# Kernel tuning notes

Hardware: AMD Instinct MI355X
Metric: run time of the kernel (lower is better)

The kernel has to match this reference:

```python
import jax, jax.numpy as jnp
import numpy as np

T, L, D, P, H = 1024, 32, 512, 512, 2048
EPS = 1e-5  # torch LayerNorm default eps


def _layer_norm(x, g, b):
    m = x.mean(axis=-1, keepdims=True)
    v = ((x - m) ** 2).mean(axis=-1, keepdims=True)
    return (x - m) * jax.lax.rsqrt(v + EPS) * g + b


def setup_inputs() -> dict:
    key = jax.random.key(0)
    ks = jax.random.split(key, 16)
    s = 0.02
    inp = {
        "base_prompts": jax.random.normal(ks[0], (T, L, D), jnp.float32),
        "new_prompt": jax.random.normal(ks[1], (L, D), jnp.float32),
        "task_embedding": jax.random.normal(ks[2], (D,), jnp.float32),
        # linear weights stored (in, out) so forward is x @ W + b
        "Wt": jax.random.normal(ks[3], (D, P), jnp.float32) * s,
        "bt": jnp.zeros((P,), jnp.float32),
        "Wq": jax.random.normal(ks[4], (D, P), jnp.float32) * s,
        "bq": jnp.zeros((P,), jnp.float32),
        "Wk": jax.random.normal(ks[5], (D, P), jnp.float32) * s,
        "bk": jnp.zeros((P,), jnp.float32),
        "Wv": jax.random.normal(ks[6], (D, P), jnp.float32) * s,
        "bv": jnp.zeros((P,), jnp.float32),
        "Wo": jax.random.normal(ks[7], (P, D), jnp.float32) * s,
        "bo": jnp.zeros((D,), jnp.float32),
        "Wa1": jax.random.normal(ks[8], (D, H), jnp.float32) * s,
        "ba1": jnp.zeros((H,), jnp.float32),
        "Wa2": jax.random.normal(ks[9], (H, D), jnp.float32) * s,
        "ba2": jnp.zeros((D,), jnp.float32),
        "g_in": jnp.ones((D,), jnp.float32),
        "b_in": jnp.zeros((D,), jnp.float32),
        "g_out": jnp.ones((D,), jnp.float32),
        "b_out": jnp.zeros((D,), jnp.float32),
    }
    return inp


def reference(base_prompts, new_prompt, task_embedding,
              Wt, bt, Wq, bq, Wk, bk, Wv, bv, Wo, bo,
              Wa1, ba1, Wa2, ba2, g_in, b_in, g_out, b_out):
    scale = 1.0 / np.sqrt(P).astype(np.float32)

    # --- task conditioning ---
    task_vec = jnp.tanh(task_embedding @ Wt + bt)                 # [P]
    key_repr = (base_prompts @ Wk + bk).mean(axis=1)              # [T,P]
    scores = (key_repr @ task_vec) * scale                        # [T]
    task_weights = jax.nn.softmax(scores)
    conditioned = base_prompts * (1.0 + task_weights[:, None, None])  # [T,L,D]

    query = new_prompt @ Wq + bq                                  # [L,P]
    keys = conditioned @ Wk + bk                                  # [T,L,P]
    values = conditioned @ Wv + bv                                # [T,L,P]

    # --- task-level attention ---
    pooled_q = query.mean(axis=0)                                 # [P]
    pooled_k = keys.mean(axis=1)                                  # [T,P]
    task_attn = jax.nn.softmax((pooled_k @ pooled_q) * scale)     # [T]
    task_weights = 0.5 * task_weights + 0.5 * task_attn
    task_weights = task_weights / jnp.maximum(task_weights.sum(), 1e-6)

    # --- enhanced mode: weighted pooling over tasks ---
    weighted_values = jnp.einsum('t,tlp->lp', task_weights, values)       # [L,P]
    weighted_keys = jnp.einsum('t,tlp->lp', task_weights, keys)           # [L,P]
    weighted_prompts = jnp.einsum('t,tld->ld', task_weights, conditioned) # [L,D]

    # --- feature-level attention ---
    feature_logits = (query @ weighted_keys.T) * scale            # [L,L]
    feature_attn = jax.nn.softmax(feature_logits, axis=-1)
    evolved_proj = feature_attn @ weighted_values                 # [L,P]

    evolved = evolved_proj @ Wo + bo                              # [L,D]
    evolved = _layer_norm(weighted_prompts + evolved, g_in, b_in)
    mlp = jax.nn.relu(evolved @ Wa1 + ba1) @ Wa2 + ba2
    aligned = _layer_norm(evolved + mlp, g_out, b_out)            # [L,D]

    aligned_prompts = jnp.broadcast_to(aligned, (T, L, D))        # stack of identical aligned prompts
    return aligned, aligned_prompts, task_weights, feature_attn
```

## Files before the change

### kernel.cpp

```cpp
#include <hip/hip_runtime.h>


typedef unsigned int u32;

static constexpr int T_ = 1024, L_ = 32, D_ = 512, P_ = 512, H_ = 2048;
static constexpr float SCALE = 0.04419417382415922f;
static constexpr float EPS_ = 1e-5f;

static constexpr int OFF_QUERY   = 0;
static constexpr int OFF_TV      = 16384;
static constexpr int OFF_PQ      = 16896;
static constexpr int OFF_WKTV    = 17408;
static constexpr int OFF_WKPQ    = 17920;
static constexpr int OFF_U       = 18432;
static constexpr int OFF_V       = 19456;
static constexpr int OFF_C       = 20480;
static constexpr int OFF_PART    = 21504;
static constexpr int OFF_WBASE   = 545792;
static constexpr int OFF_WKEY    = 562176;
static constexpr int OFF_WVAL    = 578560;
static constexpr int OFF_FA      = 594944;
static constexpr int OFF_EP      = 595968;
static constexpr int OFF_EVOLVED = 612352;
static constexpr int OFF_AQ      = 628736;
static constexpr int OFF_AKV     = 645632;
static constexpr int OFF_AEVO    = 678400;
static constexpr int OFF_AH1     = 694784;
static constexpr int OFF_AOUT    = 760320;
static constexpr int ZERO_BEGIN  = OFF_AQ;
static constexpr int ZERO_F4     = (776704 - 628736) / 4;

static constexpr int OFFO_AL = 0;
static constexpr int OFFO_AP = 16384;
static constexpr int OFFO_TW = 16384 + 16777216;
static constexpr int OFFO_FA = OFFO_TW + 1024;

__device__ __forceinline__ float wred(float v) {
    #pragma unroll
    for (int off = 32; off > 0; off >>= 1) v += __shfl_down(v, off, 64);
    return v;
}
template <int NT>
__device__ __forceinline__ float fsum(float v, float* buf, int tid) {
    v = wred(v);
    if ((tid & 63) == 0) buf[tid >> 6] = v;
    __syncthreads();
    if (tid == 0) { float s = 0.f; for (int i = 0; i < NT / 64; ++i) s += buf[i]; buf[0] = s; }
    __syncthreads();
    float r = buf[0]; __syncthreads();
    return r;
}
template <int NT>
__device__ __forceinline__ float fmaxr(float v, float* buf, int tid) {
    #pragma unroll
    for (int off = 32; off > 0; off >>= 1) v = fmaxf(v, __shfl_down(v, off, 64));
    if ((tid & 63) == 0) buf[tid >> 6] = v;
    __syncthreads();
    if (tid == 0) { float s = buf[0]; for (int i = 1; i < NT / 64; ++i) s = fmaxf(s, buf[i]); buf[0] = s; }
    __syncthreads();
    float r = buf[0]; __syncthreads();
    return r;
}

__global__ void k_zero(float* __restrict__ ws) {
    int i = blockIdx.x * 256 + threadIdx.x;
    if (i < ZERO_F4) ((float4*)(ws + ZERO_BEGIN))[i] = make_float4(0.f, 0.f, 0.f, 0.f);
}

__global__ void k_query_g(const float* __restrict__ np, const float* __restrict__ te,
                          const float* __restrict__ Wq, const float* __restrict__ Wt,
                          float* __restrict__ ws) {
    __shared__ float sx[128];
    int p = threadIdx.x, b = blockIdx.x, kc = blockIdx.y;
    const float* x = (b < L_) ? (np + b * D_) : te;
    if (p < 128) sx[p] = x[kc * 128 + p];
    __syncthreads();
    const float* W = (b < L_) ? Wq : Wt;
    float acc = 0.f;
    #pragma unroll 8
    for (int j = 0; j < 128; ++j) acc = fmaf(sx[j], W[(kc * 128 + j) * P_ + p], acc);
    atomicAdd(&ws[OFF_AQ + b * P_ + p], acc);
}

__global__ void k_query_ep(const float* __restrict__ bq, const float* __restrict__ bt,
                           float* __restrict__ ws) {
    int p = threadIdx.x, b = blockIdx.x;
    if (b < L_) ws[OFF_QUERY + b * P_ + p] = ws[OFF_AQ + b * P_ + p] + bq[p];
    else        ws[OFF_TV + p] = tanhf(ws[OFF_AQ + L_ * P_ + p] + bt[p]);
}

__global__ void k_pq(float* __restrict__ ws) {
    int p = threadIdx.x;
    float s = 0.f;
    for (int l = 0; l < L_; ++l) s += ws[OFF_QUERY + l * P_ + p];
    ws[OFF_PQ + p] = s * (1.0f / L_);
}

__global__ void k_wk2(const float* __restrict__ Wk, float* __restrict__ ws) {
    int tid = threadIdx.x, wv = tid >> 6, lane = tid & 63;
    int d = blockIdx.x * 8 + wv;
    const float4* row = (const float4*)(Wk + d * P_);
    const float4* tv4 = (const float4*)(ws + OFF_TV);
    const float4* pq4 = (const float4*)(ws + OFF_PQ);
    float4 a = row[lane * 2], b = row[lane * 2 + 1];
    float4 t0 = tv4[lane * 2], t1 = tv4[lane * 2 + 1];
    float4 q0 = pq4[lane * 2], q1 = pq4[lane * 2 + 1];
    float pa = a.x * t0.x + a.y * t0.y + a.z * t0.z + a.w * t0.w
             + b.x * t1.x + b.y * t1.y + b.z * t1.z + b.w * t1.w;
    float pb = a.x * q0.x + a.y * q0.y + a.z * q0.z + a.w * q0.w
             + b.x * q1.x + b.y * q1.y + b.z * q1.z + b.w * q1.w;
    pa = wred(pa); pb = wred(pb);
    if (lane == 0) { ws[OFF_WKTV + d] = pa; ws[OFF_WKPQ + d] = pb; }
}

__global__ void k_bbar(const float* __restrict__ base, float* __restrict__ ws) {
    __shared__ float buf[8];
    int t = blockIdx.x, d = threadIdx.x;
    const float* bp = base + (size_t)t * (L_ * D_);
    float s = 0.f;
    for (int l = 0; l < L_; ++l) s += bp[l * D_ + d];
    float up = fsum<512>(s * ws[OFF_WKTV + d], buf, d);
    float vp = fsum<512>(s * ws[OFF_WKPQ + d], buf, d);
    if (d == 0) {
        ws[OFF_U + t] = up * (1.0f / L_);
        ws[OFF_V + t] = vp * (1.0f / L_);
    }
}

__global__ void k_soft(const float* __restrict__ bk, float* __restrict__ out_tw,
                       float* __restrict__ ws) {
    __shared__ float buf[8];
    int tid = threadIdx.x;
    float pbt = 0.f, pbq = 0.f;
    for (int p = tid; p < P_; p += 256) {
        float bkf = bk[p];
        pbt = fmaf(bkf, ws[OFF_TV + p], pbt);
        pbq = fmaf(bkf, ws[OFF_PQ + p], pbq);
    }
    float bkt = fsum<256>(pbt, buf, tid);
    float bkq = fsum<256>(pbq, buf, tid);

    float s1[4], e1[4], tw1[4], lmax = -1e30f;
    #pragma unroll
    for (int k = 0; k < 4; ++k) {
        s1[k] = (ws[OFF_U + tid + k * 256] + bkt) * SCALE;
        lmax = fmaxf(lmax, s1[k]);
    }
    float gmax = fmaxr<256>(lmax, buf, tid);
    float ls = 0.f;
    #pragma unroll
    for (int k = 0; k < 4; ++k) { e1[k] = expf(s1[k] - gmax); ls += e1[k]; }
    float gs = fsum<256>(ls, buf, tid);
    #pragma unroll
    for (int k = 0; k < 4; ++k) tw1[k] = e1[k] / gs;

    float p2[4], e2[4];
    lmax = -1e30f;
    #pragma unroll
    for (int k = 0; k < 4; ++k) {
        p2[k] = ((1.0f + tw1[k]) * ws[OFF_V + tid + k * 256] + bkq) * SCALE;
        lmax = fmaxf(lmax, p2[k]);
    }
    gmax = fmaxr<256>(lmax, buf, tid);
    ls = 0.f;
    #pragma unroll
    for (int k = 0; k < 4; ++k) { e2[k] = expf(p2[k] - gmax); ls += e2[k]; }
    gs = fsum<256>(ls, buf, tid);

    float tw[4], lsum = 0.f;
    #pragma unroll
    for (int k = 0; k < 4; ++k) { tw[k] = 0.5f * tw1[k] + 0.5f * (e2[k] / gs); lsum += tw[k]; }
    float S = fsum<256>(lsum, buf, tid);
    S = fmaxf(S, 1e-6f);
    #pragma unroll
    for (int k = 0; k < 4; ++k) {
        int t = tid + k * 256;
        float twn = tw[k] / S;
        out_tw[t] = twn;
        ws[OFF_C + t] = twn * (1.0f + tw1[k]);
    }
}

__global__ void k_wpart(const float* __restrict__ base, float* __restrict__ ws) {
    __shared__ float cs[32];
    int l = blockIdx.x, ch = blockIdx.y, tid = threadIdx.x;
    if (tid < 32) cs[tid] = ws[OFF_C + ch * 32 + tid];
    __syncthreads();
    float a0 = 0.f, a1 = 0.f, a2 = 0.f, a3 = 0.f;
    for (int i = 0; i < 32; ++i) {
        int t = ch * 32 + i;
        float4 v = ((const float4*)(base + ((size_t)t * L_ + l) * D_))[tid];
        float cc = cs[i];
        a0 = fmaf(cc, v.x, a0); a1 = fmaf(cc, v.y, a1);
        a2 = fmaf(cc, v.z, a2); a3 = fmaf(cc, v.w, a3);
    }
    ((float4*)(ws + OFF_PART + (ch * L_ + l) * D_))[tid] = make_float4(a0, a1, a2, a3);
}

__global__ void k_wred(float* __restrict__ ws) {
    int l = blockIdx.x, d = threadIdx.x;
    float s = 0.f;
    for (int ch = 0; ch < 32; ++ch) s += ws[OFF_PART + (ch * L_ + l) * D_ + d];
    ws[OFF_WBASE + l * D_ + d] = s;
}

__global__ void k_wkv_g(const float* __restrict__ Wk, const float* __restrict__ Wv,
                        float* __restrict__ ws) {
    __shared__ float sx[128];
    int p = threadIdx.x, l = blockIdx.x, sel = blockIdx.y, kc = blockIdx.z;
    if (p < 128) sx[p] = ws[OFF_WBASE + l * D_ + kc * 128 + p];
    __syncthreads();
    const float* W = sel ? Wv : Wk;
    float acc = 0.f;
    #pragma unroll 8
    for (int j = 0; j < 128; ++j) acc = fmaf(sx[j], W[(kc * 128 + j) * P_ + p], acc);
    atomicAdd(&ws[OFF_AKV + (sel * L_ + l) * P_ + p], acc);
}

__global__ void k_wkv_ep(const float* __restrict__ bk, const float* __restrict__ bv,
                         float* __restrict__ ws) {
    int p = threadIdx.x, l = blockIdx.x, sel = blockIdx.y;
    float b = sel ? bv[p] : bk[p];
    ws[(sel ? OFF_WVAL : OFF_WKEY) + l * P_ + p] = ws[OFF_AKV + (sel * L_ + l) * P_ + p] + b;
}

__global__ void k_logits(float* __restrict__ out_fa, float* __restrict__ ws) {
    __shared__ __align__(16) float sq[512];
    __shared__ float lg[32];
    int l = blockIdx.x, tid = threadIdx.x, wv = tid >> 6, lane = tid & 63;
    sq[tid] = ws[OFF_QUERY + l * P_ + tid];
    __syncthreads();
    const float4* sq4 = (const float4*)sq;
    float4 q0 = sq4[lane * 2], q1 = sq4[lane * 2 + 1];
    for (int g = wv * 4; g < wv * 4 + 4; ++g) {
        const float4* kr = (const float4*)(ws + OFF_WKEY + g * P_);
        float4 a = kr[lane * 2], b = kr[lane * 2 + 1];
        float s = a.x * q0.x + a.y * q0.y + a.z * q0.z + a.w * q0.w
                + b.x * q1.x + b.y * q1.y + b.z * q1.z + b.w * q1.w;
        s = wred(s);
        if (lane == 0) lg[g] = s * SCALE;
    }
    __syncthreads();
    if (tid < 32) {
        float mx = -1e30f;
        for (int i = 0; i < 32; ++i) mx = fmaxf(mx, lg[i]);
        float S = 0.f;
        for (int i = 0; i < 32; ++i) S += expf(lg[i] - mx);
        float f = expf(lg[tid] - mx) / S;
        ws[OFF_FA + l * 32 + tid] = f;
        out_fa[l * 32 + tid] = f;
    }
}

__global__ void k_ep(float* __restrict__ ws) {
    __shared__ float fa[32];
    int l = blockIdx.x, p = threadIdx.x;
    if (p < 32) fa[p] = ws[OFF_FA + l * 32 + p];
    __syncthreads();
    float acc = 0.f;
    #pragma unroll 8
    for (int j = 0; j < L_; ++j) acc = fmaf(fa[j], ws[OFF_WVAL + j * P_ + p], acc);
    ws[OFF_EP + l * P_ + p] = acc;
}

__global__ void k_evo_g(const float* __restrict__ Wo, float* __restrict__ ws) {
    __shared__ float sx[128];
    int d = threadIdx.x, l = blockIdx.x, kc = blockIdx.y;
    if (d < 128) sx[d] = ws[OFF_EP + l * P_ + kc * 128 + d];
    __syncthreads();
    float acc = 0.f;
    #pragma unroll 8
    for (int j = 0; j < 128; ++j) acc = fmaf(sx[j], Wo[(kc * 128 + j) * D_ + d], acc);
    atomicAdd(&ws[OFF_AEVO + l * D_ + d], acc);
}

__global__ void k_xin_ln(const float* __restrict__ bo, const float* __restrict__ g_in,
                         const float* __restrict__ b_in, float* __restrict__ ws) {
    __shared__ float buf[8];
    int l = blockIdx.x, d = threadIdx.x;
    float x = ws[OFF_WBASE + l * D_ + d] + ws[OFF_AEVO + l * D_ + d] + bo[d];
    float mean = fsum<512>(x, buf, d) * (1.0f / D_);
    float dx = x - mean;
    float var = fsum<512>(dx * dx, buf, d) * (1.0f / D_);
    ws[OFF_EVOLVED + l * D_ + d] = dx * rsqrtf(var + EPS_) * g_in[d] + b_in[d];
}

__global__ void k_mlp1_g(const float* __restrict__ Wa1, float* __restrict__ ws) {
    __shared__ float sx[128];
    int tid = threadIdx.x, l = blockIdx.x, hc = blockIdx.y, kc = blockIdx.z;
    if (tid < 128) sx[tid] = ws[OFF_EVOLVED + l * D_ + kc * 128 + tid];
    __syncthreads();
    int h = hc * 512 + tid;
    float acc = 0.f;
    #pragma unroll 8
    for (int j = 0; j < 128; ++j) acc = fmaf(sx[j], Wa1[(kc * 128 + j) * H_ + h], acc);
    atomicAdd(&ws[OFF_AH1 + l * H_ + h], acc);
}

__global__ void k_mlp2_g(const float* __restrict__ Wa2, const float* __restrict__ ba1,
                         float* __restrict__ ws) {
    __shared__ float sh[128];
    int d = threadIdx.x, l = blockIdx.x, kc = blockIdx.y;
    if (d < 128) {
        int h = kc * 128 + d;
        sh[d] = fmaxf(ws[OFF_AH1 + l * H_ + h] + ba1[h], 0.f);
    }
    __syncthreads();
    float acc = 0.f;
    #pragma unroll 8
    for (int j = 0; j < 128; ++j) acc = fmaf(sh[j], Wa2[(kc * 128 + j) * D_ + d], acc);
    atomicAdd(&ws[OFF_AOUT + l * D_ + d], acc);
}

__global__ void k_lnout(const float* __restrict__ ba2, const float* __restrict__ g_out,
                        const float* __restrict__ b_out, float* __restrict__ out_al,
                        float* __restrict__ ws) {
    __shared__ float buf[8];
    int l = blockIdx.x, d = threadIdx.x;
    float x = ws[OFF_EVOLVED + l * D_ + d] + ws[OFF_AOUT + l * D_ + d] + ba2[d];
    float mean = fsum<512>(x, buf, d) * (1.0f / D_);
    float dx = x - mean;
    float var = fsum<512>(dx * dx, buf, d) * (1.0f / D_);
    out_al[l * D_ + d] = dx * rsqrtf(var + EPS_) * g_out[d] + b_out[d];
}

__global__ void k_bcast(float* __restrict__ out) {
    const float4* src = (const float4*)out;
    float4* dst = (float4*)(out + OFFO_AP);
    int idx = blockIdx.x * 256 + threadIdx.x;
    #pragma unroll
    for (int k = 0; k < 4; ++k) {
        int v = idx + k * 1048576;
        dst[v] = src[v & 4095];
    }
}

extern "C" void kernel_launch(void* const* d_in, const int* in_sizes, int n_in,
                              void* d_out, int out_size, void* d_ws, size_t ws_size,
                              hipStream_t stream) {
    const float* base = (const float*)d_in[0];
    const float* np   = (const float*)d_in[1];
    const float* te   = (const float*)d_in[2];
    const float* Wt   = (const float*)d_in[3];
    const float* bt   = (const float*)d_in[4];
    const float* Wq   = (const float*)d_in[5];
    const float* bq   = (const float*)d_in[6];
    const float* Wk   = (const float*)d_in[7];
    const float* bk   = (const float*)d_in[8];
    const float* Wv   = (const float*)d_in[9];
    const float* bv   = (const float*)d_in[10];
    const float* Wo   = (const float*)d_in[11];
    const float* bo   = (const float*)d_in[12];
    const float* Wa1  = (const float*)d_in[13];
    const float* ba1  = (const float*)d_in[14];
    const float* Wa2  = (const float*)d_in[15];
    const float* ba2  = (const float*)d_in[16];
    const float* g_in = (const float*)d_in[17];
    const float* b_in = (const float*)d_in[18];
    const float* g_out= (const float*)d_in[19];
    const float* b_out= (const float*)d_in[20];
    float* out = (float*)d_out;
    float* ws = out + OFFO_AP;

    hipLaunchKernelGGL(k_zero,     dim3(145),        dim3(256), 0, stream, ws);
    hipLaunchKernelGGL(k_query_g,  dim3(33, 4),      dim3(512), 0, stream, np, te, Wq, Wt, ws);
    hipLaunchKernelGGL(k_query_ep, dim3(33),         dim3(512), 0, stream, bq, bt, ws);
    hipLaunchKernelGGL(k_pq,       dim3(1),          dim3(512), 0, stream, ws);
    hipLaunchKernelGGL(k_wk2,      dim3(64),         dim3(512), 0, stream, Wk, ws);
    hipLaunchKernelGGL(k_bbar,     dim3(1024),       dim3(512), 0, stream, base, ws);
    hipLaunchKernelGGL(k_soft,     dim3(1),          dim3(256), 0, stream, bk, out + OFFO_TW, ws);
    hipLaunchKernelGGL(k_wpart,    dim3(32, 32),     dim3(128), 0, stream, base, ws);
    hipLaunchKernelGGL(k_wred,     dim3(32),         dim3(512), 0, stream, ws);
    hipLaunchKernelGGL(k_wkv_g,    dim3(32, 2, 4),   dim3(512), 0, stream, Wk, Wv, ws);
    hipLaunchKernelGGL(k_wkv_ep,   dim3(32, 2),      dim3(512), 0, stream, bk, bv, ws);
    hipLaunchKernelGGL(k_logits,   dim3(32),         dim3(512), 0, stream, out + OFFO_FA, ws);
    hipLaunchKernelGGL(k_ep,       dim3(32),         dim3(512), 0, stream, ws);
    hipLaunchKernelGGL(k_evo_g,    dim3(32, 4),      dim3(512), 0, stream, Wo, ws);
    hipLaunchKernelGGL(k_xin_ln,   dim3(32),         dim3(512), 0, stream, bo, g_in, b_in, ws);
    hipLaunchKernelGGL(k_mlp1_g,   dim3(32, 4, 4),   dim3(512), 0, stream, Wa1, ws);
    hipLaunchKernelGGL(k_mlp2_g,   dim3(32, 16),     dim3(512), 0, stream, Wa2, ba1, ws);
    hipLaunchKernelGGL(k_lnout,    dim3(32),         dim3(512), 0, stream, ba2, g_out, b_out, out + OFFO_AL, ws);
    hipLaunchKernelGGL(k_bcast,    dim3(4096),       dim3(256), 0, stream, out);
}
```

Before: 254.5 us.

## Fuse all stages into one cooperative persistent kernel with grid syncs

Replaces the chain of nineteen small kernel launches with a single cooperative kernel of 256 blocks that runs every stage in turn, separated by grid.sync. Atomics and the zeroing kernel go away because each GEMV block now owns its full reduction. Several stages are merged (bias folding, logits with value pooling, out-projection and layernorm), and the base-prompt sum is overlapped with the query GEMV. The aim is to cut launch overhead and inter-kernel gaps. In exchange, the small stages leave most blocks idle between grid barriers, and the large bandwidth-bound stages run on only 256 blocks.

```diff
diff --git a/kernel.cpp b/kernel.cpp
--- a/kernel.cpp
+++ b/kernel.cpp
@@ -1,337 +1,371 @@
 #include <hip/hip_runtime.h>
-
-
-typedef unsigned int u32;
+#include <hip/hip_cooperative_groups.h>
+
+
+namespace cg = cooperative_groups;
 
 static constexpr int T_ = 1024, L_ = 32, D_ = 512, P_ = 512, H_ = 2048;
 static constexpr float SCALE = 0.04419417382415922f;
 static constexpr float EPS_ = 1e-5f;
-
-static constexpr int OFF_QUERY   = 0;
-static constexpr int OFF_TV      = 16384;
-static constexpr int OFF_PQ      = 16896;
-static constexpr int OFF_WKTV    = 17408;
-static constexpr int OFF_WKPQ    = 17920;
-static constexpr int OFF_U       = 18432;
-static constexpr int OFF_V       = 19456;
-static constexpr int OFF_C       = 20480;
-static constexpr int OFF_PART    = 21504;
-static constexpr int OFF_WBASE   = 545792;
-static constexpr int OFF_WKEY    = 562176;
-static constexpr int OFF_WVAL    = 578560;
-static constexpr int OFF_FA      = 594944;
-static constexpr int OFF_EP      = 595968;
-static constexpr int OFF_EVOLVED = 612352;
-static constexpr int OFF_AQ      = 628736;
-static constexpr int OFF_AKV     = 645632;
-static constexpr int OFF_AEVO    = 678400;
-static constexpr int OFF_AH1     = 694784;
-static constexpr int OFF_AOUT    = 760320;
-static constexpr int ZERO_BEGIN  = OFF_AQ;
-static constexpr int ZERO_F4     = (776704 - 628736) / 4;
+static constexpr int NB = 256;
+static constexpr int NT = 512;
 
 static constexpr int OFFO_AL = 0;
 static constexpr int OFFO_AP = 16384;
 static constexpr int OFFO_TW = 16384 + 16777216;
 static constexpr int OFFO_FA = OFFO_TW + 1024;
 
-__device__ __forceinline__ float wred(float v) {
+static constexpr int OFF_SB      = 0;
+static constexpr int OFF_AQ      = 524288;
+static constexpr int OFF_QUERY   = 541184;
+static constexpr int OFF_TV      = 557568;
+static constexpr int OFF_PQ      = 558080;
+static constexpr int OFF_WKTV    = 558592;
+static constexpr int OFF_WKPQ    = 559104;
+static constexpr int OFF_U       = 559616;
+static constexpr int OFF_V       = 560640;
+static constexpr int OFF_C       = 561664;
+static constexpr int OFF_SC      = 562688;
+static constexpr int OFF_PART    = 562752;
+static constexpr int OFF_WB      = 693824;
+static constexpr int OFF_AKV     = 710208;
+static constexpr int OFF_EVOLVED = 742976;
+static constexpr int OFF_AH1     = 759360;
+static constexpr int OFF_AOUT    = 824896;
+
+__device__ __forceinline__ float wred64(float v) {
     #pragma unroll
     for (int off = 32; off > 0; off >>= 1) v += __shfl_down(v, off, 64);
     return v;
 }
-template <int NT>
-__device__ __forceinline__ float fsum(float v, float* buf, int tid) {
-    v = wred(v);
-    if ((tid & 63) == 0) buf[tid >> 6] = v;
-    __syncthreads();
-    if (tid == 0) { float s = 0.f; for (int i = 0; i < NT / 64; ++i) s += buf[i]; buf[0] = s; }
-    __syncthreads();
-    float r = buf[0]; __syncthreads();
-    return r;
-}
-template <int NT>
-__device__ __forceinline__ float fmaxr(float v, float* buf, int tid) {
+__device__ __forceinline__ float wmax64(float v) {
     #pragma unroll
     for (int off = 32; off > 0; off >>= 1) v = fmaxf(v, __shfl_down(v, off, 64));
+    return v;
+}
+__device__ __forceinline__ float bsum(float v, float* buf, int tid) {
+    v = wred64(v);
     if ((tid & 63) == 0) buf[tid >> 6] = v;
     __syncthreads();
-    if (tid == 0) { float s = buf[0]; for (int i = 1; i < NT / 64; ++i) s = fmaxf(s, buf[i]); buf[0] = s; }
-    __syncthreads();
-    float r = buf[0]; __syncthreads();
+    if (tid == 0) {
+        float s = 0.f;
+        #pragma unroll
+        for (int i = 0; i < 8; ++i) s += buf[i];
+        buf[0] = s;
+    }
+    __syncthreads();
+    float r = buf[0];
+    __syncthreads();
     return r;
 }
-
-__global__ void k_zero(float* __restrict__ ws) {
-    int i = blockIdx.x * 256 + threadIdx.x;
-    if (i < ZERO_F4) ((float4*)(ws + ZERO_BEGIN))[i] = make_float4(0.f, 0.f, 0.f, 0.f);
-}
-
-__global__ void k_query_g(const float* __restrict__ np, const float* __restrict__ te,
-                          const float* __restrict__ Wq, const float* __restrict__ Wt,
-                          float* __restrict__ ws) {
-    __shared__ float sx[128];
-    int p = threadIdx.x, b = blockIdx.x, kc = blockIdx.y;
-    const float* x = (b < L_) ? (np + b * D_) : te;
-    if (p < 128) sx[p] = x[kc * 128 + p];
-    __syncthreads();
-    const float* W = (b < L_) ? Wq : Wt;
-    float acc = 0.f;
-    #pragma unroll 8
-    for (int j = 0; j < 128; ++j) acc = fmaf(sx[j], W[(kc * 128 + j) * P_ + p], acc);
-    atomicAdd(&ws[OFF_AQ + b * P_ + p], acc);
-}
-
-__global__ void k_query_ep(const float* __restrict__ bq, const float* __restrict__ bt,
-                           float* __restrict__ ws) {
-    int p = threadIdx.x, b = blockIdx.x;
-    if (b < L_) ws[OFF_QUERY + b * P_ + p] = ws[OFF_AQ + b * P_ + p] + bq[p];
-    else        ws[OFF_TV + p] = tanhf(ws[OFF_AQ + L_ * P_ + p] + bt[p]);
-}
-
-__global__ void k_pq(float* __restrict__ ws) {
-    int p = threadIdx.x;
-    float s = 0.f;
-    for (int l = 0; l < L_; ++l) s += ws[OFF_QUERY + l * P_ + p];
-    ws[OFF_PQ + p] = s * (1.0f / L_);
-}
-
-__global__ void k_wk2(const float* __restrict__ Wk, float* __restrict__ ws) {
-    int tid = threadIdx.x, wv = tid >> 6, lane = tid & 63;
-    int d = blockIdx.x * 8 + wv;
-    const float4* row = (const float4*)(Wk + d * P_);
-    const float4* tv4 = (const float4*)(ws + OFF_TV);
-    const float4* pq4 = (const float4*)(ws + OFF_PQ);
-    float4 a = row[lane * 2], b = row[lane * 2 + 1];
-    float4 t0 = tv4[lane * 2], t1 = tv4[lane * 2 + 1];
-    float4 q0 = pq4[lane * 2], q1 = pq4[lane * 2 + 1];
-    float pa = a.x * t0.x + a.y * t0.y + a.z * t0.z + a.w * t0.w
-             + b.x * t1.x + b.y * t1.y + b.z * t1.z + b.w * t1.w;
-    float pb = a.x * q0.x + a.y * q0.y + a.z * q0.z + a.w * q0.w
-             + b.x * q1.x + b.y * q1.y + b.z * q1.z + b.w * q1.w;
-    pa = wred(pa); pb = wred(pb);
-    if (lane == 0) { ws[OFF_WKTV + d] = pa; ws[OFF_WKPQ + d] = pb; }
-}
-
-__global__ void k_bbar(const float* __restrict__ base, float* __restrict__ ws) {
-    __shared__ float buf[8];
-    int t = blockIdx.x, d = threadIdx.x;
-    const float* bp = base + (size_t)t * (L_ * D_);
-    float s = 0.f;
-    for (int l = 0; l < L_; ++l) s += bp[l * D_ + d];
-    float up = fsum<512>(s * ws[OFF_WKTV + d], buf, d);
-    float vp = fsum<512>(s * ws[OFF_WKPQ + d], buf, d);
-    if (d == 0) {
-        ws[OFF_U + t] = up * (1.0f / L_);
-        ws[OFF_V + t] = vp * (1.0f / L_);
-    }
-}
-
-__global__ void k_soft(const float* __restrict__ bk, float* __restrict__ out_tw,
-                       float* __restrict__ ws) {
-    __shared__ float buf[8];
-    int tid = threadIdx.x;
-    float pbt = 0.f, pbq = 0.f;
-    for (int p = tid; p < P_; p += 256) {
-        float bkf = bk[p];
-        pbt = fmaf(bkf, ws[OFF_TV + p], pbt);
-        pbq = fmaf(bkf, ws[OFF_PQ + p], pbq);
-    }
-    float bkt = fsum<256>(pbt, buf, tid);
-    float bkq = fsum<256>(pbq, buf, tid);
-
-    float s1[4], e1[4], tw1[4], lmax = -1e30f;
-    #pragma unroll
-    for (int k = 0; k < 4; ++k) {
-        s1[k] = (ws[OFF_U + tid + k * 256] + bkt) * SCALE;
-        lmax = fmaxf(lmax, s1[k]);
-    }
-    float gmax = fmaxr<256>(lmax, buf, tid);
-    float ls = 0.f;
-    #pragma unroll
-    for (int k = 0; k < 4; ++k) { e1[k] = expf(s1[k] - gmax); ls += e1[k]; }
-    float gs = fsum<256>(ls, buf, tid);
-    #pragma unroll
-    for (int k = 0; k < 4; ++k) tw1[k] = e1[k] / gs;
-
-    float p2[4], e2[4];
-    lmax = -1e30f;
-    #pragma unroll
-    for (int k = 0; k < 4; ++k) {
-        p2[k] = ((1.0f + tw1[k]) * ws[OFF_V + tid + k * 256] + bkq) * SCALE;
-        lmax = fmaxf(lmax, p2[k]);
-    }
-    gmax = fmaxr<256>(lmax, buf, tid);
-    ls = 0.f;
-    #pragma unroll
-    for (int k = 0; k < 4; ++k) { e2[k] = expf(p2[k] - gmax); ls += e2[k]; }
-    gs = fsum<256>(ls, buf, tid);
-
-    float tw[4], lsum = 0.f;
-    #pragma unroll
-    for (int k = 0; k < 4; ++k) { tw[k] = 0.5f * tw1[k] + 0.5f * (e2[k] / gs); lsum += tw[k]; }
-    float S = fsum<256>(lsum, buf, tid);
-    S = fmaxf(S, 1e-6f);
-    #pragma unroll
-    for (int k = 0; k < 4; ++k) {
-        int t = tid + k * 256;
-        float twn = tw[k] / S;
-        out_tw[t] = twn;
-        ws[OFF_C + t] = twn * (1.0f + tw1[k]);
-    }
-}
-
-__global__ void k_wpart(const float* __restrict__ base, float* __restrict__ ws) {
-    __shared__ float cs[32];
-    int l = blockIdx.x, ch = blockIdx.y, tid = threadIdx.x;
-    if (tid < 32) cs[tid] = ws[OFF_C + ch * 32 + tid];
-    __syncthreads();
-    float a0 = 0.f, a1 = 0.f, a2 = 0.f, a3 = 0.f;
-    for (int i = 0; i < 32; ++i) {
-        int t = ch * 32 + i;
-        float4 v = ((const float4*)(base + ((size_t)t * L_ + l) * D_))[tid];
-        float cc = cs[i];
-        a0 = fmaf(cc, v.x, a0); a1 = fmaf(cc, v.y, a1);
-        a2 = fmaf(cc, v.z, a2); a3 = fmaf(cc, v.w, a3);
-    }
-    ((float4*)(ws + OFF_PART + (ch * L_ + l) * D_))[tid] = make_float4(a0, a1, a2, a3);
-}
-
-__global__ void k_wred(float* __restrict__ ws) {
-    int l = blockIdx.x, d = threadIdx.x;
-    float s = 0.f;
-    for (int ch = 0; ch < 32; ++ch) s += ws[OFF_PART + (ch * L_ + l) * D_ + d];
-    ws[OFF_WBASE + l * D_ + d] = s;
-}
-
-__global__ void k_wkv_g(const float* __restrict__ Wk, const float* __restrict__ Wv,
-                        float* __restrict__ ws) {
-    __shared__ float sx[128];
-    int p = threadIdx.x, l = blockIdx.x, sel = blockIdx.y, kc = blockIdx.z;
-    if (p < 128) sx[p] = ws[OFF_WBASE + l * D_ + kc * 128 + p];
-    __syncthreads();
-    const float* W = sel ? Wv : Wk;
-    float acc = 0.f;
-    #pragma unroll 8
-    for (int j = 0; j < 128; ++j) acc = fmaf(sx[j], W[(kc * 128 + j) * P_ + p], acc);
-    atomicAdd(&ws[OFF_AKV + (sel * L_ + l) * P_ + p], acc);
-}
-
-__global__ void k_wkv_ep(const float* __restrict__ bk, const float* __restrict__ bv,
-                         float* __restrict__ ws) {
-    int p = threadIdx.x, l = blockIdx.x, sel = blockIdx.y;
-    float b = sel ? bv[p] : bk[p];
-    ws[(sel ? OFF_WVAL : OFF_WKEY) + l * P_ + p] = ws[OFF_AKV + (sel * L_ + l) * P_ + p] + b;
-}
-
-__global__ void k_logits(float* __restrict__ out_fa, float* __restrict__ ws) {
-    __shared__ __align__(16) float sq[512];
-    __shared__ float lg[32];
-    int l = blockIdx.x, tid = threadIdx.x, wv = tid >> 6, lane = tid & 63;
-    sq[tid] = ws[OFF_QUERY + l * P_ + tid];
-    __syncthreads();
-    const float4* sq4 = (const float4*)sq;
-    float4 q0 = sq4[lane * 2], q1 = sq4[lane * 2 + 1];
-    for (int g = wv * 4; g < wv * 4 + 4; ++g) {
-        const float4* kr = (const float4*)(ws + OFF_WKEY + g * P_);
-        float4 a = kr[lane * 2], b = kr[lane * 2 + 1];
-        float s = a.x * q0.x + a.y * q0.y + a.z * q0.z + a.w * q0.w
-                + b.x * q1.x + b.y * q1.y + b.z * q1.z + b.w * q1.w;
-        s = wred(s);
-        if (lane == 0) lg[g] = s * SCALE;
-    }
-    __syncthreads();
-    if (tid < 32) {
-        float mx = -1e30f;
-        for (int i = 0; i < 32; ++i) mx = fmaxf(mx, lg[i]);
-        float S = 0.f;
-        for (int i = 0; i < 32; ++i) S += expf(lg[i] - mx);
-        float f = expf(lg[tid] - mx) / S;
-        ws[OFF_FA + l * 32 + tid] = f;
-        out_fa[l * 32 + tid] = f;
-    }
-}
-
-__global__ void k_ep(float* __restrict__ ws) {
-    __shared__ float fa[32];
-    int l = blockIdx.x, p = threadIdx.x;
-    if (p < 32) fa[p] = ws[OFF_FA + l * 32 + p];
-    __syncthreads();
-    float acc = 0.f;
-    #pragma unroll 8
-    for (int j = 0; j < L_; ++j) acc = fmaf(fa[j], ws[OFF_WVAL + j * P_ + p], acc);
-    ws[OFF_EP + l * P_ + p] = acc;
-}
-
-__global__ void k_evo_g(const float* __restrict__ Wo, float* __restrict__ ws) {
-    __shared__ float sx[128];
-    int d = threadIdx.x, l = blockIdx.x, kc = blockIdx.y;
-    if (d < 128) sx[d] = ws[OFF_EP + l * P_ + kc * 128 + d];
-    __syncthreads();
-    float acc = 0.f;
-    #pragma unroll 8
-    for (int j = 0; j < 128; ++j) acc = fmaf(sx[j], Wo[(kc * 128 + j) * D_ + d], acc);
-    atomicAdd(&ws[OFF_AEVO + l * D_ + d], acc);
-}
-
-__global__ void k_xin_ln(const float* __restrict__ bo, const float* __restrict__ g_in,
-                         const float* __restrict__ b_in, float* __restrict__ ws) {
-    __shared__ float buf[8];
-    int l = blockIdx.x, d = threadIdx.x;
-    float x = ws[OFF_WBASE + l * D_ + d] + ws[OFF_AEVO + l * D_ + d] + bo[d];
-    float mean = fsum<512>(x, buf, d) * (1.0f / D_);
-    float dx = x - mean;
-    float var = fsum<512>(dx * dx, buf, d) * (1.0f / D_);
-    ws[OFF_EVOLVED + l * D_ + d] = dx * rsqrtf(var + EPS_) * g_in[d] + b_in[d];
-}
-
-__global__ void k_mlp1_g(const float* __restrict__ Wa1, float* __restrict__ ws) {
-    __shared__ float sx[128];
-    int tid = threadIdx.x, l = blockIdx.x, hc = blockIdx.y, kc = blockIdx.z;
-    if (tid < 128) sx[tid] = ws[OFF_EVOLVED + l * D_ + kc * 128 + tid];
-    __syncthreads();
-    int h = hc * 512 + tid;
-    float acc = 0.f;
-    #pragma unroll 8
-    for (int j = 0; j < 128; ++j) acc = fmaf(sx[j], Wa1[(kc * 128 + j) * H_ + h], acc);
-    atomicAdd(&ws[OFF_AH1 + l * H_ + h], acc);
-}
-
-__global__ void k_mlp2_g(const float* __restrict__ Wa2, const float* __restrict__ ba1,
-                         float* __restrict__ ws) {
-    __shared__ float sh[128];
-    int d = threadIdx.x, l = blockIdx.x, kc = blockIdx.y;
-    if (d < 128) {
-        int h = kc * 128 + d;
-        sh[d] = fmaxf(ws[OFF_AH1 + l * H_ + h] + ba1[h], 0.f);
-    }
-    __syncthreads();
-    float acc = 0.f;
-    #pragma unroll 8
-    for (int j = 0; j < 128; ++j) acc = fmaf(sh[j], Wa2[(kc * 128 + j) * D_ + d], acc);
-    atomicAdd(&ws[OFF_AOUT + l * D_ + d], acc);
-}
-
-__global__ void k_lnout(const float* __restrict__ ba2, const float* __restrict__ g_out,
-                        const float* __restrict__ b_out, float* __restrict__ out_al,
-                        float* __restrict__ ws) {
-    __shared__ float buf[8];
-    int l = blockIdx.x, d = threadIdx.x;
-    float x = ws[OFF_EVOLVED + l * D_ + d] + ws[OFF_AOUT + l * D_ + d] + ba2[d];
-    float mean = fsum<512>(x, buf, d) * (1.0f / D_);
-    float dx = x - mean;
-    float var = fsum<512>(dx * dx, buf, d) * (1.0f / D_);
-    out_al[l * D_ + d] = dx * rsqrtf(var + EPS_) * g_out[d] + b_out[d];
-}
-
-__global__ void k_bcast(float* __restrict__ out) {
-    const float4* src = (const float4*)out;
-    float4* dst = (float4*)(out + OFFO_AP);
-    int idx = blockIdx.x * 256 + threadIdx.x;
-    #pragma unroll
-    for (int k = 0; k < 4; ++k) {
-        int v = idx + k * 1048576;
-        dst[v] = src[v & 4095];
+__device__ __forceinline__ float bmax(float v, float* buf, int tid) {
+    v = wmax64(v);
+    if ((tid & 63) == 0) buf[tid >> 6] = v;
+    __syncthreads();
+    if (tid == 0) {
+        float s = buf[0];
+        #pragma unroll
+        for (int i = 1; i < 8; ++i) s = fmaxf(s, buf[i]);
+        buf[0] = s;
+    }
+    __syncthreads();
+    float r = buf[0];
+    __syncthreads();
+    return r;
+}
+
+__global__ __launch_bounds__(512, 2) void mega(
+    const float* __restrict__ base, const float* __restrict__ np_,
+    const float* __restrict__ te,   const float* __restrict__ Wq,
+    const float* __restrict__ Wt,   const float* __restrict__ bq,
+    const float* __restrict__ bt,   const float* __restrict__ Wk,
+    const float* __restrict__ bk,   const float* __restrict__ Wv,
+    const float* __restrict__ bv,   const float* __restrict__ Wo,
+    const float* __restrict__ bo,   const float* __restrict__ Wa1,
+    const float* __restrict__ ba1,  const float* __restrict__ Wa2,
+    const float* __restrict__ ba2,  const float* __restrict__ g_in,
+    const float* __restrict__ b_in, const float* __restrict__ g_out,
+    const float* __restrict__ b_out, float* __restrict__ out)
+{
+    cg::grid_group grid = cg::this_grid();
+    __shared__ __align__(16) float smem[2560];
+    float* ws = out + OFFO_AP;
+    const int blk = blockIdx.x, tid = threadIdx.x;
+
+    if (blk < 33) {
+        const float* x = (blk < 32) ? (np_ + blk * D_) : te;
+        const float* W = (blk < 32) ? Wq : Wt;
+        smem[tid] = x[tid];
+        __syncthreads();
+        float acc = 0.f;
+        #pragma unroll 8
+        for (int j = 0; j < D_; ++j) acc = fmaf(smem[j], W[j * P_ + tid], acc);
+        ws[OFF_AQ + blk * P_ + tid] = acc;
+    } else {
+        for (int t = blk - 33; t < T_; t += NB - 33) {
+            const float* bp = base + (size_t)t * (L_ * D_);
+            float s = 0.f;
+            #pragma unroll
+            for (int l = 0; l < L_; ++l) s += bp[l * D_ + tid];
+            ws[OFF_SB + t * D_ + tid] = s;
+        }
+    }
+    grid.sync();
+
+    if (blk < 32) {
+        ws[OFF_QUERY + blk * P_ + tid] = ws[OFF_AQ + blk * P_ + tid] + bq[tid];
+    } else if (blk == 32) {
+        ws[OFF_TV + tid] = tanhf(ws[OFF_AQ + 32 * P_ + tid] + bt[tid]);
+    } else if (blk == 33) {
+        float s = 0.f;
+        #pragma unroll
+        for (int l = 0; l < L_; ++l) s += ws[OFF_AQ + l * P_ + tid];
+        ws[OFF_PQ + tid] = s * (1.f / L_) + bq[tid];
+    }
+    grid.sync();
+
+    if (blk < 64) {
+        int wv = tid >> 6, lane = tid & 63;
+        int d = blk * 8 + wv;
+        const float4* row = (const float4*)(Wk + d * P_);
+        const float4* tv4 = (const float4*)(ws + OFF_TV);
+        const float4* pq4 = (const float4*)(ws + OFF_PQ);
+        float4 a = row[lane * 2], b = row[lane * 2 + 1];
+        float4 t0 = tv4[lane * 2], t1 = tv4[lane * 2 + 1];
+        float4 q0 = pq4[lane * 2], q1 = pq4[lane * 2 + 1];
+        float pa = a.x * t0.x + a.y * t0.y + a.z * t0.z + a.w * t0.w
+                 + b.x * t1.x + b.y * t1.y + b.z * t1.z + b.w * t1.w;
+        float pb = a.x * q0.x + a.y * q0.y + a.z * q0.z + a.w * q0.w
+                 + b.x * q1.x + b.y * q1.y + b.z * q1.z + b.w * q1.w;
+        pa = wred64(pa); pb = wred64(pb);
+        if (lane == 0) { ws[OFF_WKTV + d] = pa; ws[OFF_WKPQ + d] = pb; }
+    } else if (blk == 64) {
+        float pbt = bk[tid] * ws[OFF_TV + tid];
+        float pbq = bk[tid] * ws[OFF_PQ + tid];
+        pbt = bsum(pbt, smem, tid);
+        pbq = bsum(pbq, smem, tid);
+        if (tid == 0) { ws[OFF_SC] = pbt; ws[OFF_SC + 1] = pbq; }
+    }
+    grid.sync();
+
+    for (int t = blk; t < T_; t += NB) {
+        float sb = ws[OFF_SB + t * D_ + tid];
+        float a = bsum(sb * ws[OFF_WKTV + tid], smem, tid);
+        float b = bsum(sb * ws[OFF_WKPQ + tid], smem, tid);
+        if (tid == 0) {
+            ws[OFF_U + t] = a * (1.f / L_);
+            ws[OFF_V + t] = b * (1.f / L_);
+        }
+    }
+    grid.sync();
+
+    if (blk == 0) {
+        float* buf = smem;
+        float bkt = ws[OFF_SC], bkq = ws[OFF_SC + 1];
+        float s1[2], e1[2], tw1[2];
+        float lmax = -1e30f;
+        #pragma unroll
+        for (int k = 0; k < 2; ++k) {
+            s1[k] = (ws[OFF_U + tid + k * NT] + bkt) * SCALE;
+            lmax = fmaxf(lmax, s1[k]);
+        }
+        float gmax = bmax(lmax, buf, tid);
+        float ls = 0.f;
+        #pragma unroll
+        for (int k = 0; k < 2; ++k) { e1[k] = expf(s1[k] - gmax); ls += e1[k]; }
+        float gs = bsum(ls, buf, tid);
+        #pragma unroll
+        for (int k = 0; k < 2; ++k) tw1[k] = e1[k] / gs;
+
+        float p2[2], e2[2];
+        lmax = -1e30f;
+        #pragma unroll
+        for (int k = 0; k < 2; ++k) {
+            p2[k] = ((1.f + tw1[k]) * ws[OFF_V + tid + k * NT] + bkq) * SCALE;
+            lmax = fmaxf(lmax, p2[k]);
+        }
+        gmax = bmax(lmax, buf, tid);
+        ls = 0.f;
+        #pragma unroll
+        for (int k = 0; k < 2; ++k) { e2[k] = expf(p2[k] - gmax); ls += e2[k]; }
+        gs = bsum(ls, buf, tid);
+
+        float tw[2], lsum = 0.f;
+        #pragma unroll
+        for (int k = 0; k < 2; ++k) {
+            tw[k] = 0.5f * tw1[k] + 0.5f * (e2[k] / gs);
+            lsum += tw[k];
+        }
+        float S = bsum(lsum, buf, tid);
+        S = fmaxf(S, 1e-6f);
+        #pragma unroll
+        for (int k = 0; k < 2; ++k) {
+            int t = tid + k * NT;
+            float twn = tw[k] / S;
+            out[OFFO_TW + t] = twn;
+            ws[OFF_C + t] = twn * (1.f + tw1[k]);
+        }
+    }
+    grid.sync();
+
+    {
+        int l = blk & 31, ch = blk >> 5;
+        int d4 = tid & 127, tq = tid >> 7;
+        float* sc = smem + 2048;
+        if (tid < 128) sc[tid] = ws[OFF_C + ch * 128 + tid];
+        __syncthreads();
+        float4 acc = make_float4(0.f, 0.f, 0.f, 0.f);
+        for (int i = tq; i < 128; i += 4) {
+            int t = ch * 128 + i;
+            float c = sc[i];
+            float4 v = ((const float4*)(base + ((size_t)t * L_ + l) * D_))[d4];
+            acc.x = fmaf(c, v.x, acc.x);
+            acc.y = fmaf(c, v.y, acc.y);
+            acc.z = fmaf(c, v.z, acc.z);
+            acc.w = fmaf(c, v.w, acc.w);
+        }
+        float4* s4 = (float4*)smem;
+        s4[tid] = acc;
+        __syncthreads();
+        if (tid < 128) {
+            float4 a = s4[tid], b = s4[tid + 128], c2 = s4[tid + 256], d2 = s4[tid + 384];
+            float4 r;
+            r.x = a.x + b.x + c2.x + d2.x;
+            r.y = a.y + b.y + c2.y + d2.y;
+            r.z = a.z + b.z + c2.z + d2.z;
+            r.w = a.w + b.w + c2.w + d2.w;
+            ((float4*)(ws + OFF_PART + (ch * 32 + l) * D_))[tid] = r;
+        }
+    }
+    grid.sync();
+
+    if (blk < 64) {
+        int l = blk >> 1, sel = blk & 1;
+        float s = 0.f;
+        #pragma unroll
+        for (int ch = 0; ch < 8; ++ch) s += ws[OFF_PART + (ch * 32 + l) * D_ + tid];
+        smem[tid] = s;
+        if (sel == 0) ws[OFF_WB + l * D_ + tid] = s;
+        __syncthreads();
+        const float* W = sel ? Wv : Wk;
+        float acc = 0.f;
+        #pragma unroll 8
+        for (int j = 0; j < D_; ++j) acc = fmaf(smem[j], W[j * P_ + tid], acc);
+        ws[OFF_AKV + (sel * L_ + l) * P_ + tid] = acc;
+    }
+    grid.sync();
+
+    if (blk < 32) {
+        int l = blk;
+        float* sq  = smem;
+        float* slg = smem + 512;
+        float* sfa = smem + 544;
+        float* sep = smem + 576;
+        float* buf = smem + 1088;
+        sq[tid] = ws[OFF_QUERY + l * P_ + tid];
+        __syncthreads();
+        int wv = tid >> 6, lane = tid & 63;
+        const float4* sq4 = (const float4*)sq;
+        const float4* bk4 = (const float4*)bk;
+        float4 q0 = sq4[lane * 2], q1 = sq4[lane * 2 + 1];
+        float4 kb0 = bk4[lane * 2], kb1 = bk4[lane * 2 + 1];
+        #pragma unroll
+        for (int gi = 0; gi < 4; ++gi) {
+            int g = wv * 4 + gi;
+            const float4* kr = (const float4*)(ws + OFF_AKV + g * P_);
+            float4 a = kr[lane * 2], b = kr[lane * 2 + 1];
+            float s = (a.x + kb0.x) * q0.x + (a.y + kb0.y) * q0.y
+                    + (a.z + kb0.z) * q0.z + (a.w + kb0.w) * q0.w
+                    + (b.x + kb1.x) * q1.x + (b.y + kb1.y) * q1.y
+                    + (b.z + kb1.z) * q1.z + (b.w + kb1.w) * q1.w;
+            s = wred64(s);
+            if (lane == 0) slg[g] = s * SCALE;
+        }
+        __syncthreads();
+        if (tid < 32) {
+            float mx = -1e30f;
+            for (int i = 0; i < 32; ++i) mx = fmaxf(mx, slg[i]);
+            float S = 0.f;
+            for (int i = 0; i < 32; ++i) S += expf(slg[i] - mx);
+            float f = expf(slg[tid] - mx) / S;
+            sfa[tid] = f;
+            out[OFFO_FA + l * 32 + tid] = f;
+        }
+        __syncthreads();
+        float bvp = bv[tid];
+        float acc = 0.f;
+        #pragma unroll 8
+        for (int j = 0; j < L_; ++j)
+            acc = fmaf(sfa[j], ws[OFF_AKV + (L_ + j) * P_ + tid] + bvp, acc);
+        sep[tid] = acc;
+        __syncthreads();
+        float ev = 0.f;
+        #pragma unroll 8
+        for (int j = 0; j < D_; ++j) ev = fmaf(sep[j], Wo[j * D_ + tid], ev);
+        float x = ws[OFF_WB + l * D_ + tid] + ev + bo[tid];
+        float mean = bsum(x, buf, tid) * (1.f / D_);
+        float dx = x - mean;
+        float var = bsum(dx * dx, buf, tid) * (1.f / D_);
+        ws[OFF_EVOLVED + l * D_ + tid] = dx * rsqrtf(var + EPS_) * g_in[tid] + b_in[tid];
+    }
+    grid.sync();
+
+    if (blk < 128) {
+        int l = blk >> 2, hc = blk & 3;
+        smem[tid] = ws[OFF_EVOLVED + l * D_ + tid];
+        __syncthreads();
+        int h = hc * 512 + tid;
+        float acc = 0.f;
+        #pragma unroll 8
+        for (int j = 0; j < D_; ++j) acc = fmaf(smem[j], Wa1[j * H_ + h], acc);
+        ws[OFF_AH1 + l * H_ + h] = acc;
+    }
+    grid.sync();
+
+    if (blk < 128) {
+        int l = blk >> 2, dq = blk & 3;
+        float* sx  = smem;
+        float* buf = smem + 2048;
+        #pragma unroll
+        for (int k = 0; k < 4; ++k) {
+            int h = k * 512 + tid;
+            sx[h] = fmaxf(ws[OFF_AH1 + l * H_ + h] + ba1[h], 0.f);
+        }
+        __syncthreads();
+        int col = tid & 127, ks = tid >> 7;
+        int d = dq * 128 + col;
+        int j0 = ks * 512;
+        float acc = 0.f;
+        #pragma unroll 8
+        for (int j = j0; j < j0 + 512; ++j) acc = fmaf(sx[j], Wa2[j * D_ + d], acc);
+        buf[tid] = acc;
+        __syncthreads();
+        if (tid < 128) {
+            float s = buf[tid] + buf[tid + 128] + buf[tid + 256] + buf[tid + 384];
+            ws[OFF_AOUT + l * D_ + dq * 128 + tid] = s;
+        }
+    }
+    grid.sync();
+
+    if (blk < 32) {
+        int l = blk;
+        float x = ws[OFF_EVOLVED + l * D_ + tid] + ws[OFF_AOUT + l * D_ + tid] + ba2[tid];
+        float mean = bsum(x, smem, tid) * (1.f / D_);
+        float dx = x - mean;
+        float var = bsum(dx * dx, smem, tid) * (1.f / D_);
+        out[OFFO_AL + l * D_ + tid] = dx * rsqrtf(var + EPS_) * g_out[tid] + b_out[tid];
+    }
+    grid.sync();
+
+    {
+        const float4* src = (const float4*)out;
+        float4* dst = (float4*)(out + OFFO_AP);
+        int idx = blk * NT + tid;
+        #pragma unroll
+        for (int k = 0; k < 32; ++k) {
+            int v = idx + k * (NB * NT);
+            dst[v] = src[v & 4095];
+        }
     }
 }
 
@@ -360,25 +394,14 @@
     const float* g_out= (const float*)d_in[19];
     const float* b_out= (const float*)d_in[20];
     float* out = (float*)d_out;
-    float* ws = out + OFFO_AP;
-
-    hipLaunchKernelGGL(k_zero,     dim3(145),        dim3(256), 0, stream, ws);
-    hipLaunchKernelGGL(k_query_g,  dim3(33, 4),      dim3(512), 0, stream, np, te, Wq, Wt, ws);
-    hipLaunchKernelGGL(k_query_ep, dim3(33),         dim3(512), 0, stream, bq, bt, ws);
-    hipLaunchKernelGGL(k_pq,       dim3(1),          dim3(512), 0, stream, ws);
-    hipLaunchKernelGGL(k_wk2,      dim3(64),         dim3(512), 0, stream, Wk, ws);
-    hipLaunchKernelGGL(k_bbar,     dim3(1024),       dim3(512), 0, stream, base, ws);
-    hipLaunchKernelGGL(k_soft,     dim3(1),          dim3(256), 0, stream, bk, out + OFFO_TW, ws);
-    hipLaunchKernelGGL(k_wpart,    dim3(32, 32),     dim3(128), 0, stream, base, ws);
-    hipLaunchKernelGGL(k_wred,     dim3(32),         dim3(512), 0, stream, ws);
-    hipLaunchKernelGGL(k_wkv_g,    dim3(32, 2, 4),   dim3(512), 0, stream, Wk, Wv, ws);
-    hipLaunchKernelGGL(k_wkv_ep,   dim3(32, 2),      dim3(512), 0, stream, bk, bv, ws);
-    hipLaunchKernelGGL(k_logits,   dim3(32),         dim3(512), 0, stream, out + OFFO_FA, ws);
-    hipLaunchKernelGGL(k_ep,       dim3(32),         dim3(512), 0, stream, ws);
-    hipLaunchKernelGGL(k_evo_g,    dim3(32, 4),      dim3(512), 0, stream, Wo, ws);
-    hipLaunchKernelGGL(k_xin_ln,   dim3(32),         dim3(512), 0, stream, bo, g_in, b_in, ws);
-    hipLaunchKernelGGL(k_mlp1_g,   dim3(32, 4, 4),   dim3(512), 0, stream, Wa1, ws);
-    hipLaunchKernelGGL(k_mlp2_g,   dim3(32, 16),     dim3(512), 0, stream, Wa2, ba1, ws);
-    hipLaunchKernelGGL(k_lnout,    dim3(32),         dim3(512), 0, stream, ba2, g_out, b_out, out + OFFO_AL, ws);
-    hipLaunchKernelGGL(k_bcast,    dim3(4096),       dim3(256), 0, stream, out);
-}
+
+    void* args[] = {
+        (void*)&base, (void*)&np, (void*)&te, (void*)&Wq, (void*)&Wt,
+        (void*)&bq, (void*)&bt, (void*)&Wk, (void*)&bk, (void*)&Wv,
+        (void*)&bv, (void*)&Wo, (void*)&bo, (void*)&Wa1, (void*)&ba1,
+        (void*)&Wa2, (void*)&ba2, (void*)&g_in, (void*)&b_in, (void*)&g_out,
+        (void*)&b_out, (void*)&out
+    };
+    hipLaunchCooperativeKernel((const void*)mega, dim3(NB), dim3(NT),
+                               args, 0, stream);
+}
```

After: 658.8 us. +158.9%, slower.
